# Optimization experiments

Measured on AMD Instinct MI355X. Metric: run time of the kernel, lower is better.

## Reference

```python
import jax, jax.numpy as jnp
import numpy as np

B, S, D = 2, 1024, 1024
L, E, F = 2, 8, 2048


def setup_inputs() -> dict:
    key = jax.random.key(0)
    kx, kp, k1, k2 = jax.random.split(key, 4)
    x = jax.random.normal(kx, (B, S, D), dtype=jnp.float32)
    # prototypes scaled so dot products are O(1), keeping softmax well-behaved
    protos = jax.random.normal(kp, (L, E, D), dtype=jnp.float32) / np.sqrt(D)
    W1 = jax.random.normal(k1, (L, E, D, F), dtype=jnp.float32) * 0.02
    W2 = jax.random.normal(k2, (L, E, F, D), dtype=jnp.float32) * 0.02
    return {"x": x, "protos": protos, "W1": W1, "W2": W2, "k": 2}


def _route(x, protos_l, k):
    # expert_mapping: abs(dot(prototype, input)) per expert, keep top-k, rest -> -inf, softmax
    scores = jnp.abs(jnp.einsum("bsd,ed->bse", x, protos_l))  # [B,S,E]
    topv, _ = jax.lax.top_k(scores, k)
    thresh = topv[..., -1:]  # k-th largest per token
    masked = jnp.where(scores >= thresh, scores, -jnp.inf)
    return jax.nn.softmax(masked, axis=-1)  # [B,S,E]


def reference(x, protos, W1, W2, k):
    n_layers = protos.shape[0]
    for l in range(n_layers):  # fixed small layer loop
        w = _route(x, protos[l], k)  # [B,S,E]
        h = jax.nn.relu(jnp.einsum("bsd,edf->bsef", x, W1[l]))  # [B,S,E,F]
        y = jnp.einsum("bsef,efd,bse->bsd", h, W2[l], w)  # weighted expert mix
        x = x + y
    return x
```

## Files before the change

### kernel.cpp

```cpp
#include <hip/hip_runtime.h>
#include <hip/hip_bf16.h>
#include <cstdint>

#define T_TOKENS 2048
#define DDIM 1024
#define FDIM 2048
#define NEXP 8
#define BMPAD 64
#define RMAX 4608
#define RALLOC 4736

#define ATILE_EL 2048
#define BTILE_EL 4096

typedef unsigned short u16;
typedef short bf16x8 __attribute__((ext_vector_type(8)));
typedef u16 u16x8 __attribute__((ext_vector_type(8)));
typedef u16 u16x4v __attribute__((ext_vector_type(4)));
typedef float f32x4 __attribute__((ext_vector_type(4)));

#define VMCNT(n) asm volatile("s_waitcnt vmcnt(" #n ")" ::: "memory")
#define SB() __builtin_amdgcn_sched_barrier(0)
#define BAR() __builtin_amdgcn_s_barrier()

__device__ __forceinline__ u16 bf16_rn(float f) {
  unsigned u = __builtin_bit_cast(unsigned, f);
  u += 0x7fffu + ((u >> 16) & 1u);
  return (u16)(u >> 16);
}
__device__ __forceinline__ float bf16_f(u16 h) {
  unsigned u = ((unsigned)h) << 16;
  return __builtin_bit_cast(float, u);
}
__device__ __forceinline__ void gl16(const void* g, void* l) {
  __builtin_amdgcn_global_load_lds((const __attribute__((address_space(1))) void*)g,
                                   (__attribute__((address_space(3))) void*)l, 16, 0, 0);
}

template <int GX, int GY, int GZ>
__device__ __forceinline__ void swz3(unsigned lin, int& bx, int& by, int& bz) {
  constexpr unsigned nwg = (unsigned)GX * GY * GZ;
  const unsigned nl = (lin & 7u) * (nwg >> 3) + (lin >> 3);
  bx = nl % GX;
  const unsigned t = nl / GX;
  by = t % GY;
  bz = t / GY;
}


__device__ __forceinline__ void route_dev(
    int t, const float* __restrict__ x, const float* __restrict__ protos,
    int* __restrict__ eid, float* __restrict__ wgt, float* red) {
  const int tid = threadIdx.x;
  const float4 xv = ((const float4*)(x + (size_t)t * DDIM))[tid];
  float acc[NEXP];
#pragma unroll
  for (int e = 0; e < NEXP; ++e) {
    const float4 p = ((const float4*)protos)[e * 256 + tid];
    acc[e] = xv.x * p.x + xv.y * p.y + xv.z * p.z + xv.w * p.w;
  }
#pragma unroll
  for (int e = 0; e < NEXP; ++e) red[e * 256 + tid] = acc[e];
  __syncthreads();
  for (int s = 128; s > 0; s >>= 1) {
    if (tid < s) {
#pragma unroll
      for (int e = 0; e < NEXP; ++e) red[e * 256 + tid] += red[e * 256 + tid + s];
    }
    __syncthreads();
  }
  if (tid == 0) {
    float m1 = -1.f, m2 = -1.f;
    int i1 = 0, i2 = 0;
#pragma unroll
    for (int e = 0; e < NEXP; ++e) {
      float s = fabsf(red[e * 256]);
      if (s > m1) { m2 = m1; i2 = i1; m1 = s; i1 = e; }
      else if (s > m2) { m2 = s; i2 = e; }
    }
    float e2 = __expf(m2 - m1);
    float z = 1.f + e2;
    eid[t * 2] = i1;
    eid[t * 2 + 1] = i2;
    wgt[t * 2] = 1.f / z;
    wgt[t * 2 + 1] = e2 / z;
  }
}

template <bool LO>
__device__ __forceinline__ void wconv_dev(
    int nb, int kb, int e, const float* __restrict__ W, u16* __restrict__ Hi,
    u16* __restrict__ Lo, int K, int N, float* tile) {
  const float* Wp = W + ((size_t)e * K + (size_t)kb * 32) * N + nb * 128;
  const int t = threadIdx.x;
#pragma unroll
  for (int i = 0; i < 4; ++i) {
    const int f4 = i * 256 + t;
    const int kr = f4 >> 5;
    const int c4 = (f4 & 31) * 4;
    float4 v = *(const float4*)(Wp + (size_t)kr * N + c4);
    *(float4*)&tile[kr * 129 + c4] = v;
  }
  __syncthreads();
  const size_t tb = (((size_t)e * (N >> 7) + nb) * (K >> 5) + kb) * BTILE_EL;
#pragma unroll
  for (int j = 0; j < 2; ++j) {
    const int cid = j * 256 + t;
    const int n = cid & 127, ksel = cid >> 7;
    u16x8 hv, lv;
#pragma unroll
    for (int i = 0; i < 8; ++i) {
      float f = tile[(ksel * 8 + i) * 129 + n];
      u16 h = bf16_rn(f);
      hv[i] = h;
      if (LO) lv[i] = bf16_rn(f - bf16_f(h));
    }
    *(u16x8*)(Hi + tb + (size_t)cid * 8) = hv;
    if (LO) *(u16x8*)(Lo + tb + (size_t)cid * 8) = lv;
  }
}

__device__ __forceinline__ void wconv_p_dev(
    int nb, int kb, int e, const float* __restrict__ W, u16* __restrict__ Hi,
    const float* __restrict__ proto2, float* __restrict__ Ppart, int K, int N,
    float* smem) {
  float* tile = smem;
  float* pr = smem + 32 * 129;
  const float* Wp = W + ((size_t)e * K + (size_t)kb * 32) * N + nb * 128;
  const int t = threadIdx.x;
#pragma unroll
  for (int i = 0; i < 4; ++i) {
    const int f4 = i * 256 + t;
    const int kr = f4 >> 5;
    const int c4 = (f4 & 31) * 4;
    float4 v = *(const float4*)(Wp + (size_t)kr * N + c4);
    *(float4*)&tile[kr * 129 + c4] = v;
  }
  {
    const int idx = t * 4;
    const int e2 = idx >> 7, n = idx & 127;
    *(float4*)&pr[e2 * 128 + n] =
        *(const float4*)(proto2 + (size_t)e2 * DDIM + nb * 128 + n);
  }
  __syncthreads();
  const size_t tb = (((size_t)e * (N >> 7) + nb) * (K >> 5) + kb) * BTILE_EL;
#pragma unroll
  for (int j = 0; j < 2; ++j) {
    const int cid = j * 256 + t;
    const int n = cid & 127, ksel = cid >> 7;
    u16x8 hv;
#pragma unroll
    for (int i = 0; i < 8; ++i) hv[i] = bf16_rn(tile[(ksel * 8 + i) * 129 + n]);
    *(u16x8*)(Hi + tb + (size_t)cid * 8) = hv;
  }
  const int e2 = t >> 5, f = t & 31;
  float s = 0.f;
#pragma unroll 16
  for (int n = 0; n < 128; ++n) s += tile[f * 129 + n] * pr[e2 * 128 + n];
  Ppart[(((size_t)nb * NEXP + e) * NEXP + e2) * FDIM + kb * 32 + f] = s;
}

template <bool LO>
__device__ __forceinline__ void gather_dev(
    int r, const float* __restrict__ x, const int* __restrict__ row2token,
    u16* __restrict__ Ahi, u16* __restrict__ Alo) {
  const int t = row2token[r];
  const int c = threadIdx.x * 4;
  float4 v = make_float4(0.f, 0.f, 0.f, 0.f);
  if (t >= 0) v = *(const float4*)(x + (size_t)t * DDIM + c);
  float vv[4] = {v.x, v.y, v.z, v.w};
  u16x4v hi, lo;
#pragma unroll
  for (int i = 0; i < 4; ++i) {
    u16 h = bf16_rn(vv[i]);
    hi[i] = h;
    if (LO) lo[i] = bf16_rn(vv[i] - bf16_f(h));
  }
  const size_t el = ((size_t)(r >> 6) * (DDIM >> 5) + (c >> 5)) * ATILE_EL +
                    (size_t)(((c >> 3) & 3) * 64 + (r & 63)) * 8 + (c & 7);
  *(u16x4v*)(Ahi + el) = hi;
  if (LO) *(u16x4v*)(Alo + el) = lo;
}

__device__ __forceinline__ void gemm_split_dev(
    unsigned lin, u16* lds, const u16* __restrict__ Ahi, const u16* __restrict__ Alo,
    const u16* __restrict__ Bhi, const u16* __restrict__ Blo,
    u16* __restrict__ OutHi, u16* __restrict__ OutLo,
    const int* __restrict__ cnt, const int* __restrict__ offp, int K, int N) {
  int bx, by, bz;
  swz3<FDIM / 128, RMAX / 64, NEXP>(lin, bx, by, bz);
  const int e = bz;
  const int cp = (cnt[e] + 63) & ~63;
  if (by * 64 >= cp) return;
  const int row0 = offp[e] + by * 64;
  const int n0 = bx * 128;
  const int nkb = K >> 5;
  constexpr int BUF_EL = 12288;

  const int tid = threadIdx.x;
  const int lane = tid & 63;
  const int wid = tid >> 6;
  const int wr = wid >> 1, wc = wid & 1;
  const int lr = lane & 15, kg = lane >> 4;
  const int lo16 = lane << 4;

  f32x4 acc[2][4];
#pragma unroll
  for (int i = 0; i < 2; ++i)
#pragma unroll
    for (int j = 0; j < 4; ++j)
#pragma unroll
      for (int r = 0; r < 4; ++r) acc[i][j][r] = 0.f;

  const size_t abase = (size_t)(row0 >> 6) * nkb;
  const size_t bbase = ((size_t)e * (N >> 7) + (n0 >> 7)) * nkb;

  auto STAGE = [&](int kb, int b) {
    char* d = (char*)(lds + b * BUF_EL);
    const char* gah = (const char*)(Ahi + (abase + kb) * ATILE_EL);
    const char* gal = (const char*)(Alo + (abase + kb) * ATILE_EL);
    const char* gbh = (const char*)(Bhi + (bbase + kb) * BTILE_EL);
    const char* gbl = (const char*)(Blo + (bbase + kb) * BTILE_EL);
    if (wid == 0) {
      gl16(gah + 0 * 1024 + lo16, d + 0 * 1024);
      gl16(gah + 1 * 1024 + lo16, d + 1 * 1024);
      gl16(gah + 2 * 1024 + lo16, d + 2 * 1024);
      gl16(gah + 3 * 1024 + lo16, d + 3 * 1024);
      gl16(gal + 0 * 1024 + lo16, d + 4096 + 0 * 1024);
      gl16(gal + 1 * 1024 + lo16, d + 4096 + 1 * 1024);
    } else if (wid == 1) {
      gl16(gal + 2 * 1024 + lo16, d + 4096 + 2 * 1024);
      gl16(gal + 3 * 1024 + lo16, d + 4096 + 3 * 1024);
      gl16(gbh + 0 * 1024 + lo16, d + 8192 + 0 * 1024);
      gl16(gbh + 1 * 1024 + lo16, d + 8192 + 1 * 1024);
      gl16(gbh + 2 * 1024 + lo16, d + 8192 + 2 * 1024);
      gl16(gbh + 3 * 1024 + lo16, d + 8192 + 3 * 1024);
    } else if (wid == 2) {
      gl16(gbh + 4 * 1024 + lo16, d + 8192 + 4 * 1024);
      gl16(gbh + 5 * 1024 + lo16, d + 8192 + 5 * 1024);
      gl16(gbh + 6 * 1024 + lo16, d + 8192 + 6 * 1024);
      gl16(gbh + 7 * 1024 + lo16, d + 8192 + 7 * 1024);
      gl16(gbl + 0 * 1024 + lo16, d + 16384 + 0 * 1024);
      gl16(gbl + 1 * 1024 + lo16, d + 16384 + 1 * 1024);
    } else {
      gl16(gbl + 2 * 1024 + lo16, d + 16384 + 2 * 1024);
      gl16(gbl + 3 * 1024 + lo16, d + 16384 + 3 * 1024);
      gl16(gbl + 4 * 1024 + lo16, d + 16384 + 4 * 1024);
      gl16(gbl + 5 * 1024 + lo16, d + 16384 + 5 * 1024);
      gl16(gbl + 6 * 1024 + lo16, d + 16384 + 6 * 1024);
      gl16(gbl + 7 * 1024 + lo16, d + 16384 + 7 * 1024);
    }
  };

  STAGE(0, 0);
  int cur = 0;
  for (int kb = 0; kb < nkb; ++kb) {
    const bool pf = (kb + 1 < nkb);
    if (pf) STAGE(kb + 1, cur ^ 1);
    if (pf) { VMCNT(6); } else { VMCNT(0); }
    SB(); BAR(); SB();

    const u16* buf = lds + cur * BUF_EL;
    const u16* AsH = buf;
    const u16* AsL = buf + 2048;
    const u16* BsH = buf + 4096;
    const u16* BsL = buf + 8192;
    const int arow = (kg * 64 + wr * 32 + lr) * 8;
    const int bcol = (kg * 128 + wc * 64 + lr) * 8;

    bf16x8 ah0 = *(const bf16x8*)&AsH[arow];
    bf16x8 ah1 = *(const bf16x8*)&AsH[arow + 128];
    bf16x8 bh[4];
#pragma unroll
    for (int j = 0; j < 4; ++j) bh[j] = *(const bf16x8*)&BsH[bcol + j * 128];
#pragma unroll
    for (int j = 0; j < 4; ++j) {
      acc[0][j] = __builtin_amdgcn_mfma_f32_16x16x32_bf16(ah0, bh[j], acc[0][j], 0, 0, 0);
      acc[1][j] = __builtin_amdgcn_mfma_f32_16x16x32_bf16(ah1, bh[j], acc[1][j], 0, 0, 0);
    }
    bf16x8 al0 = *(const bf16x8*)&AsL[arow];
    bf16x8 al1 = *(const bf16x8*)&AsL[arow + 128];
#pragma unroll
    for (int j = 0; j < 4; ++j) {
      bf16x8 bl = *(const bf16x8*)&BsL[bcol + j * 128];
      acc[0][j] = __builtin_amdgcn_mfma_f32_16x16x32_bf16(ah0, bl, acc[0][j], 0, 0, 0);
      acc[1][j] = __builtin_amdgcn_mfma_f32_16x16x32_bf16(ah1, bl, acc[1][j], 0, 0, 0);
      acc[0][j] = __builtin_amdgcn_mfma_f32_16x16x32_bf16(al0, bh[j], acc[0][j], 0, 0, 0);
      acc[1][j] = __builtin_amdgcn_mfma_f32_16x16x32_bf16(al1, bh[j], acc[1][j], 0, 0, 0);
    }
    SB(); BAR(); SB();
    cur ^= 1;
  }

  const int nkbO = N >> 5;
#pragma unroll
  for (int i = 0; i < 2; ++i) {
#pragma unroll
    for (int j = 0; j < 4; ++j) {
      const int Cj = n0 + wc * 64 + j * 16 + lr;
      f32x4 v = acc[i][j];
#pragma unroll
      for (int r = 0; r < 4; ++r) {
        const int R = row0 + wr * 32 + i * 16 + kg * 4 + r;
        float f = fmaxf(v[r], 0.f);
        const size_t el = ((size_t)(R >> 6) * nkbO + (Cj >> 5)) * ATILE_EL +
                          (size_t)(((Cj >> 3) & 3) * 64 + (R & 63)) * 8 + (Cj & 7);
        u16 h = bf16_rn(f);
        OutHi[el] = h;
        OutLo[el] = bf16_rn(f - bf16_f(h));
      }
    }
  }
}

template <int GX, int GY, bool RELU, int OUTMODE>
__device__ __forceinline__ void gemm_plain_dev(
    unsigned lin, u16* lds, const u16* __restrict__ Ahi, const u16* __restrict__ Bhi,
    u16* __restrict__ OutHi, float* __restrict__ OutF,
    const int* __restrict__ cnt, const int* __restrict__ offp, int K, int N) {
  int bx, by, bz;
  swz3<GX, GY, NEXP>(lin, bx, by, bz);
  const int e = bz;
  const int cp = (cnt[e] + 63) & ~63;
  if (by * 128 >= cp) return;
  const int row0 = offp[e] + by * 128;
  const int rend = offp[e] + cp;
  const int n0 = bx * 128;
  const int nkb = K >> 5;
  constexpr int BUF_EL = 8192;

  const int tid = threadIdx.x;
  const int lane = tid & 63;
  const int wid = tid >> 6;
  const int wr = wid >> 1, wc = wid & 1;
  const int lr = lane & 15, kg = lane >> 4;
  const int lo16 = lane << 4;

  f32x4 acc[4][4];
#pragma unroll
  for (int i = 0; i < 4; ++i)
#pragma unroll
    for (int j = 0; j < 4; ++j)
#pragma unroll
      for (int r = 0; r < 4; ++r) acc[i][j][r] = 0.f;

  const int at0 = row0 >> 6;
  const size_t bbase = ((size_t)e * (N >> 7) + (n0 >> 7)) * nkb;

  auto STAGE = [&](int kb, int b) {
    char* d = (char*)(lds + b * BUF_EL);
    if (wid < 2) {
      const char* g = (const char*)(Ahi + ((size_t)(at0 + wid) * nkb + kb) * ATILE_EL);
      gl16(g + 0 * 1024 + lo16, d + wid * 4096 + 0 * 1024);
      gl16(g + 1 * 1024 + lo16, d + wid * 4096 + 1 * 1024);
      gl16(g + 2 * 1024 + lo16, d + wid * 4096 + 2 * 1024);
      gl16(g + 3 * 1024 + lo16, d + wid * 4096 + 3 * 1024);
    } else {
      const char* g = (const char*)(Bhi + (bbase + kb) * BTILE_EL) + (wid - 2) * 4096;
      gl16(g + 0 * 1024 + lo16, d + 8192 + (wid - 2) * 4096 + 0 * 1024);
      gl16(g + 1 * 1024 + lo16, d + 8192 + (wid - 2) * 4096 + 1 * 1024);
      gl16(g + 2 * 1024 + lo16, d + 8192 + (wid - 2) * 4096 + 2 * 1024);
      gl16(g + 3 * 1024 + lo16, d + 8192 + (wid - 2) * 4096 + 3 * 1024);
    }
  };

  STAGE(0, 0);
  int cur = 0;
  for (int kb = 0; kb < nkb; ++kb) {
    const bool pf = (kb + 1 < nkb);
    if (pf) STAGE(kb + 1, cur ^ 1);
    if (pf) { VMCNT(4); } else { VMCNT(0); }
    SB(); BAR(); SB();

    const u16* buf = lds + cur * BUF_EL;
    const u16* AsH = buf + wr * 2048;
    const u16* BsH = buf + 4096;
    const int arow = (kg * 64 + lr) * 8;
    const int bcol = (kg * 128 + wc * 64 + lr) * 8;

    bf16x8 ah[4], bh[4];
#pragma unroll
    for (int i = 0; i < 4; ++i) ah[i] = *(const bf16x8*)&AsH[arow + i * 128];
#pragma unroll
    for (int j = 0; j < 4; ++j) bh[j] = *(const bf16x8*)&BsH[bcol + j * 128];
#pragma unroll
    for (int i = 0; i < 4; ++i)
#pragma unroll
      for (int j = 0; j < 4; ++j)
        acc[i][j] = __builtin_amdgcn_mfma_f32_16x16x32_bf16(ah[i], bh[j], acc[i][j], 0, 0, 0);
    SB(); BAR(); SB();
    cur ^= 1;
  }

  const int nkbO = N >> 5;
#pragma unroll
  for (int i = 0; i < 4; ++i) {
#pragma unroll
    for (int j = 0; j < 4; ++j) {
      const int Cj = n0 + wc * 64 + j * 16 + lr;
      f32x4 v = acc[i][j];
#pragma unroll
      for (int r = 0; r < 4; ++r) {
        const int R = row0 + wr * 64 + i * 16 + kg * 4 + r;
        if (R >= rend) continue;
        float f = v[r];
        if (RELU) f = fmaxf(f, 0.f);
        if constexpr (OUTMODE == 0) {
          OutF[(size_t)R * N + Cj] = f;
        } else {
          const size_t el = ((size_t)(R >> 6) * nkbO + (Cj >> 5)) * ATILE_EL +
                            (size_t)(((Cj >> 3) & 3) * 64 + (R & 63)) * 8 + (Cj & 7);
          OutHi[el] = bf16_rn(f);
        }
      }
    }
  }
}

__device__ __forceinline__ void compact_dev(
    const int* __restrict__ eid, int* __restrict__ cnt, int* __restrict__ offp,
    int* __restrict__ row2token, int* __restrict__ pos, int* lcnt) {
  int* s_off = lcnt + NEXP * 256;
  int* s_tot = s_off + NEXP;
  const int tid = threadIdx.x;
  const int base = tid * 16;
  int my[16];
#pragma unroll
  for (int i = 0; i < 4; ++i)
    *(int4*)&my[i * 4] = *(const int4*)(eid + base + i * 4);
#pragma unroll
  for (int e = 0; e < NEXP; ++e) {
    int c = 0;
#pragma unroll
    for (int i = 0; i < 16; ++i) c += (my[i] == e) ? 1 : 0;
    lcnt[e * 256 + tid] = c;
  }
  for (int r = tid; r < RMAX; r += 256) row2token[r] = -1;
  __syncthreads();
  if (tid < NEXP) {
    int run = 0;
    for (int i = 0; i < 256; ++i) {
      int v = lcnt[tid * 256 + i];
      lcnt[tid * 256 + i] = run;
      run += v;
    }
    s_tot[tid] = run;
  }
  __syncthreads();
  if (tid == 0) {
    int o = 0;
    for (int e = 0; e < NEXP; ++e) {
      s_off[e] = o;
      o += (s_tot[e] + BMPAD - 1) & ~(BMPAD - 1);
    }
  }
  __syncthreads();
  int myoff[NEXP];
#pragma unroll
  for (int e = 0; e < NEXP; ++e) myoff[e] = s_off[e] + lcnt[e * 256 + tid];
#pragma unroll
  for (int i = 0; i < 16; ++i) {
    int r = 0;
#pragma unroll
    for (int e = 0; e < NEXP; ++e) r = (my[i] == e) ? myoff[e] : r;
    row2token[r] = (base + i) >> 1;
    pos[base + i] = r;
#pragma unroll
    for (int e = 0; e < NEXP; ++e) myoff[e] += (my[i] == e) ? 1 : 0;
  }
  if (tid < NEXP) {
    cnt[tid] = s_tot[tid];
    offp[tid] = s_off[tid];
  }
}


__global__ __launch_bounds__(256) void fusedK1_kernel(
    const float* __restrict__ xin, const float* __restrict__ protos,
    int* __restrict__ eidA, float* __restrict__ wgtA,
    const float* __restrict__ W2, u16* __restrict__ W2A,
    const float* __restrict__ proto2, float* __restrict__ Ppart,
    const float* __restrict__ W1, u16* __restrict__ W_hi, u16* __restrict__ W_lo) {
  __shared__ float smem[32 * 129 + 8 * 128];
  const unsigned lin = blockIdx.x;
  if (lin < 2048u) {
    route_dev((int)lin, xin, protos, eidA, wgtA, smem);
  } else if (lin < 6144u) {
    const unsigned l2 = lin - 2048u;
    wconv_p_dev(l2 % 8, (l2 / 8) % 64, l2 / 512, W2, W2A, proto2, Ppart,
                FDIM, DDIM, smem);
  } else {
    const unsigned l3 = lin - 6144u;
    wconv_dev<true>(l3 % 16, (l3 / 16) % 32, l3 / 512, W1, W_hi, W_lo,
                    DDIM, FDIM, smem);
  }
}

__global__ __launch_bounds__(256) void compact_kernel(
    const int* __restrict__ eid, int* __restrict__ cnt, int* __restrict__ offp,
    int* __restrict__ row2token, int* __restrict__ pos) {
  __shared__ int lcnt[NEXP * 256 + 16];
  compact_dev(eid, cnt, offp, row2token, pos, lcnt);
}

__global__ __launch_bounds__(256) void fusedK3_kernel(
    const float* __restrict__ xin, const int* __restrict__ row2token,
    u16* __restrict__ Ag_hi, u16* __restrict__ Ag_lo,
    const float* __restrict__ Ppart, float* __restrict__ P) {
  const unsigned lin = blockIdx.x;
  if (lin < (unsigned)RMAX) {
    gather_dev<true>((int)lin, xin, row2token, Ag_hi, Ag_lo);
  } else {
    const int i = (int)(lin - RMAX) * 256 + threadIdx.x;
    float s = 0.f;
#pragma unroll
    for (int nb = 0; nb < 8; ++nb) s += Ppart[(size_t)nb * (NEXP * NEXP * FDIM) + i];
    P[i] = s;
  }
}

__global__ __launch_bounds__(256, 3) void fusedC2_kernel(
    const u16* __restrict__ Ag_hi, const u16* __restrict__ Ag_lo,
    const u16* __restrict__ W_hi, const u16* __restrict__ W_lo,
    u16* __restrict__ h_hi, u16* __restrict__ h_lo,
    const int* __restrict__ cnt, const int* __restrict__ offp) {
  __shared__ u16 lds[2 * 12288];
  gemm_split_dev(blockIdx.x, lds, Ag_hi, Ag_lo, W_hi, W_lo, h_hi, h_lo, cnt, offp,
                 DDIM, FDIM);
}

__global__ __launch_bounds__(256, 4) void fusedC3_kernel(
    const u16* __restrict__ h_hi, const u16* __restrict__ W2A,
    float* __restrict__ part, const int* __restrict__ cnt, const int* __restrict__ offp,
    const float* __restrict__ W1b, u16* __restrict__ W_lo,
    const float* __restrict__ W2b, u16* __restrict__ W_hi) {
  __shared__ u16 lds[2 * 8192];
  const unsigned lin = blockIdx.x;
  if (lin < 2304u) {
    gemm_plain_dev<DDIM / 128, RMAX / 128, false, 0>(
        lin, lds, h_hi, W2A, nullptr, part, cnt, offp, FDIM, DDIM);
  } else if (lin < 6400u) {
    const unsigned l2 = lin - 2304u;
    wconv_dev<false>(l2 % 16, (l2 / 16) % 32, l2 / 512, W1b, W_lo, nullptr,
                     DDIM, FDIM, (float*)lds);
  } else {
    const unsigned l2 = lin - 6400u;
    wconv_dev<false>(l2 % 8, (l2 / 8) % 64, l2 / 512, W2b, W_hi, nullptr,
                     FDIM, DDIM, (float*)lds);
  }
}

__global__ __launch_bounds__(256) void route2_kernel(
    const float* __restrict__ x, const float* __restrict__ protos2,
    const u16* __restrict__ h_hi, const u16* __restrict__ h_lo,
    const float* __restrict__ P, const int* __restrict__ eidA,
    const int* __restrict__ pos, const float* __restrict__ wgtA,
    int* __restrict__ eidB, float* __restrict__ wgtB) {
  const int t = blockIdx.x;
  const int tid = threadIdx.x;
  __shared__ float red[NEXP][256];
  const float4 xv = ((const float4*)(x + (size_t)t * DDIM))[tid];
  float acc[NEXP];
#pragma unroll
  for (int e = 0; e < NEXP; ++e) {
    const float4 p = ((const float4*)protos2)[e * 256 + tid];
    acc[e] = xv.x * p.x + xv.y * p.y + xv.z * p.z + xv.w * p.w;
  }
  const int p0 = pos[t * 2], p1 = pos[t * 2 + 1];
  const int e0 = eidA[t * 2], e1 = eidA[t * 2 + 1];
  const float w0 = wgtA[t * 2], w1 = wgtA[t * 2 + 1];
  const int f0 = tid * 8;
  const int nkbF = FDIM >> 5;
  float h0[8], h1[8];
  {
    const size_t el0 = ((size_t)(p0 >> 6) * nkbF + (f0 >> 5)) * ATILE_EL +
                       (size_t)((((f0 >> 3) & 3) * 64 + (p0 & 63)) * 8);
    const size_t el1 = ((size_t)(p1 >> 6) * nkbF + (f0 >> 5)) * ATILE_EL +
                       (size_t)((((f0 >> 3) & 3) * 64 + (p1 & 63)) * 8);
    u16x8 a = *(const u16x8*)&h_hi[el0], b = *(const u16x8*)&h_lo[el0];
    u16x8 c = *(const u16x8*)&h_hi[el1], d = *(const u16x8*)&h_lo[el1];
#pragma unroll
    for (int j = 0; j < 8; ++j) {
      h0[j] = bf16_f(a[j]) + bf16_f(b[j]);
      h1[j] = bf16_f(c[j]) + bf16_f(d[j]);
    }
  }
#pragma unroll
  for (int e2 = 0; e2 < NEXP; ++e2) {
    const float* P0 = P + ((size_t)(e0 * NEXP + e2)) * FDIM + f0;
    const float* P1 = P + ((size_t)(e1 * NEXP + e2)) * FDIM + f0;
    float c = 0.f;
#pragma unroll
    for (int j = 0; j < 8; ++j) c += w0 * h0[j] * P0[j] + w1 * h1[j] * P1[j];
    acc[e2] += c;
  }
#pragma unroll
  for (int e = 0; e < NEXP; ++e) red[e][tid] = acc[e];
  __syncthreads();
  for (int s = 128; s > 0; s >>= 1) {
    if (tid < s) {
#pragma unroll
      for (int e = 0; e < NEXP; ++e) red[e][tid] += red[e][tid + s];
    }
    __syncthreads();
  }
  if (tid == 0) {
    float m1 = -1.f, m2 = -1.f;
    int i1 = 0, i2 = 0;
#pragma unroll
    for (int e = 0; e < NEXP; ++e) {
      float s = fabsf(red[e][0]);
      if (s > m1) { m2 = m1; i2 = i1; m1 = s; i1 = e; }
      else if (s > m2) { m2 = s; i2 = e; }
    }
    float e2 = __expf(m2 - m1);
    float z = 1.f + e2;
    eidB[t * 2] = i1;
    eidB[t * 2 + 1] = i2;
    wgtB[t * 2] = 1.f / z;
    wgtB[t * 2 + 1] = e2 / z;
  }
}

__global__ __launch_bounds__(256) void fusedD_kernel(
    const float* __restrict__ part, const int* __restrict__ pos,
    const float* __restrict__ wgt, const float* __restrict__ xin,
    float* __restrict__ xcur,
    const int* __restrict__ eidB, int* __restrict__ cnt, int* __restrict__ offp,
    int* __restrict__ row2token, int* __restrict__ posB) {
  __shared__ int lcnt[NEXP * 256 + 16];
  const unsigned lin = blockIdx.x;
  if (lin < 2048u) {
    const int t = lin;
    const int c = threadIdx.x * 4;
    const int p0 = pos[t * 2], p1 = pos[t * 2 + 1];
    const float w0 = wgt[t * 2], w1 = wgt[t * 2 + 1];
    float4 xa = *(const float4*)(xin + (size_t)t * DDIM + c);
    const float4 y0 = *(const float4*)(part + (size_t)p0 * DDIM + c);
    const float4 y1 = *(const float4*)(part + (size_t)p1 * DDIM + c);
    xa.x += w0 * y0.x + w1 * y1.x;
    xa.y += w0 * y0.y + w1 * y1.y;
    xa.z += w0 * y0.z + w1 * y1.z;
    xa.w += w0 * y0.w + w1 * y1.w;
    *(float4*)(xcur + (size_t)t * DDIM + c) = xa;
  } else {
    compact_dev(eidB, cnt, offp, row2token, posB, lcnt);
  }
}

__global__ __launch_bounds__(256) void gather_kernel(
    const float* __restrict__ x, const int* __restrict__ row2token,
    u16* __restrict__ Ahi) {
  gather_dev<false>(blockIdx.x, x, row2token, Ahi, nullptr);
}

template <int GX, bool RELU, int OUTMODE>
__global__ __launch_bounds__(256, 4) void gemm_plain_kernel(
    const u16* __restrict__ Ahi, const u16* __restrict__ Bhi,
    u16* __restrict__ OutHi, float* __restrict__ OutF,
    const int* __restrict__ cnt, const int* __restrict__ offp, int K, int N) {
  __shared__ u16 lds[2 * 8192];
  gemm_plain_dev<GX, RMAX / 128, RELU, OUTMODE>(blockIdx.x, lds, Ahi, Bhi, OutHi,
                                                OutF, cnt, offp, K, N);
}

__global__ __launch_bounds__(256) void apply_kernel(
    const float* __restrict__ part, const int* __restrict__ pos,
    const float* __restrict__ wgt, float* __restrict__ x) {
  const int t = blockIdx.x;
  const int c = threadIdx.x * 4;
  const int p0 = pos[t * 2], p1 = pos[t * 2 + 1];
  const float w0 = wgt[t * 2], w1 = wgt[t * 2 + 1];
  float4 xa = *(float4*)(x + (size_t)t * DDIM + c);
  const float4 y0 = *(const float4*)(part + (size_t)p0 * DDIM + c);
  const float4 y1 = *(const float4*)(part + (size_t)p1 * DDIM + c);
  xa.x += w0 * y0.x + w1 * y1.x;
  xa.y += w0 * y0.y + w1 * y1.y;
  xa.z += w0 * y0.z + w1 * y1.z;
  xa.w += w0 * y0.w + w1 * y1.w;
  *(float4*)(x + (size_t)t * DDIM + c) = xa;
}

extern "C" void kernel_launch(void* const* d_in, const int* in_sizes, int n_in,
                              void* d_out, int out_size, void* d_ws, size_t ws_size,
                              hipStream_t stream) {
  const float* xin = (const float*)d_in[0];
  const float* protos = (const float*)d_in[1];
  const float* W1 = (const float*)d_in[2];
  const float* W2 = (const float*)d_in[3];
  float* xcur = (float*)d_out;

  u16* W_hi = (u16*)d_ws;
  u16* W_lo = W_hi + (size_t)NEXP * DDIM * FDIM;
  u16* W2A = W_lo + (size_t)NEXP * DDIM * FDIM;
  u16* Ag_hi = W2A + (size_t)NEXP * DDIM * FDIM;
  u16* Ag_lo = Ag_hi + (size_t)RALLOC * DDIM;
  u16* h_hi = Ag_lo + (size_t)RALLOC * DDIM;
  u16* h_lo = h_hi + (size_t)RALLOC * FDIM;
  float* part = (float*)(h_lo + (size_t)RALLOC * FDIM);
  float* Ppart = part + (size_t)RALLOC * DDIM;
  float* P = Ppart + (size_t)8 * NEXP * NEXP * FDIM;
  float* wgtA = P + (size_t)NEXP * NEXP * FDIM;
  float* wgtB = wgtA + T_TOKENS * 2;
  int* eidA = (int*)(wgtB + T_TOKENS * 2);
  int* eidB = eidA + T_TOKENS * 2;
  int* posA = eidB + T_TOKENS * 2;
  int* posB = posA + T_TOKENS * 2;
  int* cnt = posB + T_TOKENS * 2;
  int* offp = cnt + NEXP;
  int* row2token = offp + NEXP;

  const float* protos2 = protos + (size_t)NEXP * DDIM;
  const float* W1b = W1 + (size_t)NEXP * DDIM * FDIM;
  const float* W2b = W2 + (size_t)NEXP * FDIM * DDIM;

  fusedK1_kernel<<<2048 + 4096 + 4096, 256, 0, stream>>>(
      xin, protos, eidA, wgtA, W2, W2A, protos2, Ppart, W1, W_hi, W_lo);
  compact_kernel<<<1, 256, 0, stream>>>(eidA, cnt, offp, row2token, posA);
  fusedK3_kernel<<<RMAX + 512, 256, 0, stream>>>(
      xin, row2token, Ag_hi, Ag_lo, Ppart, P);
  fusedC2_kernel<<<(FDIM / 128) * (RMAX / 64) * NEXP, 256, 0, stream>>>(
      Ag_hi, Ag_lo, W_hi, W_lo, h_hi, h_lo, cnt, offp);
  fusedC3_kernel<<<2304 + 4096 + 4096, 256, 0, stream>>>(
      h_hi, W2A, part, cnt, offp, W1b, W_lo, W2b, W_hi);
  route2_kernel<<<T_TOKENS, 256, 0, stream>>>(
      xin, protos2, h_hi, h_lo, P, eidA, posA, wgtA, eidB, wgtB);
  fusedD_kernel<<<2048 + 1, 256, 0, stream>>>(
      part, posA, wgtA, xin, xcur, eidB, cnt, offp, row2token, posB);

  gather_kernel<<<RMAX, 256, 0, stream>>>(xcur, row2token, Ag_hi);
  gemm_plain_kernel<FDIM / 128, true, 2>
      <<<(FDIM / 128) * (RMAX / 128) * NEXP, 256, 0, stream>>>(
          Ag_hi, W_lo, h_hi, nullptr, cnt, offp, DDIM, FDIM);
  gemm_plain_kernel<DDIM / 128, false, 0>
      <<<(DDIM / 128) * (RMAX / 128) * NEXP, 256, 0, stream>>>(
          h_hi, W_hi, nullptr, part, cnt, offp, FDIM, DDIM);
  apply_kernel<<<T_TOKENS, 256, 0, stream>>>(part, posB, wgtB, xcur);
}
```

Before: 331.3 us.

## Fuse second-layer routing into C3 kernel and fix LDS padding in weight conversion

Moves the route2 kernel's work into extra blocks of fusedC3, removing one kernel launch and letting routing run alongside the GEMM and weight-conversion blocks. It also changes the weight-transpose LDS row pitch from 129 to 132 floats so float4 stores are aligned. The proto dot product is rewritten with float4 reads whose start index is rotated per thread to spread LDS bank accesses. Cost: the shared 16K-u16 LDS buffer (32 KB) must hold route2's 8x256 float reduction array, and fusedC3 gets more parameters and register pressure.

```diff
diff --git a/kernel.cpp b/kernel.cpp
--- a/kernel.cpp
+++ b/kernel.cpp
@@ -12,6 +12,7 @@
 
 #define ATILE_EL 2048
 #define BTILE_EL 4096
+#define WLDP 132
 
 typedef unsigned short u16;
 typedef short bf16x8 __attribute__((ext_vector_type(8)));
@@ -99,7 +100,7 @@
     const int kr = f4 >> 5;
     const int c4 = (f4 & 31) * 4;
     float4 v = *(const float4*)(Wp + (size_t)kr * N + c4);
-    *(float4*)&tile[kr * 129 + c4] = v;
+    *(float4*)&tile[kr * WLDP + c4] = v;
   }
   __syncthreads();
   const size_t tb = (((size_t)e * (N >> 7) + nb) * (K >> 5) + kb) * BTILE_EL;
@@ -110,7 +111,7 @@
     u16x8 hv, lv;
 #pragma unroll
     for (int i = 0; i < 8; ++i) {
-      float f = tile[(ksel * 8 + i) * 129 + n];
+      float f = tile[(ksel * 8 + i) * WLDP + n];
       u16 h = bf16_rn(f);
       hv[i] = h;
       if (LO) lv[i] = bf16_rn(f - bf16_f(h));
@@ -125,7 +126,7 @@
     const float* __restrict__ proto2, float* __restrict__ Ppart, int K, int N,
     float* smem) {
   float* tile = smem;
-  float* pr = smem + 32 * 129;
+  float* pr = smem + 32 * WLDP;
   const float* Wp = W + ((size_t)e * K + (size_t)kb * 32) * N + nb * 128;
   const int t = threadIdx.x;
 #pragma unroll
@@ -134,7 +135,7 @@
     const int kr = f4 >> 5;
     const int c4 = (f4 & 31) * 4;
     float4 v = *(const float4*)(Wp + (size_t)kr * N + c4);
-    *(float4*)&tile[kr * 129 + c4] = v;
+    *(float4*)&tile[kr * WLDP + c4] = v;
   }
   {
     const int idx = t * 4;
@@ -150,13 +151,18 @@
     const int n = cid & 127, ksel = cid >> 7;
     u16x8 hv;
 #pragma unroll
-    for (int i = 0; i < 8; ++i) hv[i] = bf16_rn(tile[(ksel * 8 + i) * 129 + n]);
+    for (int i = 0; i < 8; ++i) hv[i] = bf16_rn(tile[(ksel * 8 + i) * WLDP + n]);
     *(u16x8*)(Hi + tb + (size_t)cid * 8) = hv;
   }
   const int e2 = t >> 5, f = t & 31;
   float s = 0.f;
-#pragma unroll 16
-  for (int n = 0; n < 128; ++n) s += tile[f * 129 + n] * pr[e2 * 128 + n];
+#pragma unroll
+  for (int ii = 0; ii < 32; ++ii) {
+    const int n4 = ((ii + f) & 31) * 4;
+    const float4 tv = *(const float4*)&tile[f * WLDP + n4];
+    const float4 pv = *(const float4*)&pr[e2 * 128 + n4];
+    s += tv.x * pv.x + tv.y * pv.y + tv.z * pv.z + tv.w * pv.w;
+  }
   Ppart[(((size_t)nb * NEXP + e) * NEXP + e2) * FDIM + kb * 32 + f] = s;
 }
 
@@ -180,6 +186,76 @@
                     (size_t)(((c >> 3) & 3) * 64 + (r & 63)) * 8 + (c & 7);
   *(u16x4v*)(Ahi + el) = hi;
   if (LO) *(u16x4v*)(Alo + el) = lo;
+}
+
+__device__ __forceinline__ void route2_dev(
+    int t, const float* __restrict__ x, const float* __restrict__ protos2,
+    const u16* __restrict__ h_hi, const u16* __restrict__ h_lo,
+    const float* __restrict__ P, const int* __restrict__ eidA,
+    const int* __restrict__ pos, const float* __restrict__ wgtA,
+    int* __restrict__ eidB, float* __restrict__ wgtB, float* red) {
+  const int tid = threadIdx.x;
+  const float4 xv = ((const float4*)(x + (size_t)t * DDIM))[tid];
+  float acc[NEXP];
+#pragma unroll
+  for (int e = 0; e < NEXP; ++e) {
+    const float4 p = ((const float4*)protos2)[e * 256 + tid];
+    acc[e] = xv.x * p.x + xv.y * p.y + xv.z * p.z + xv.w * p.w;
+  }
+  const int p0 = pos[t * 2], p1 = pos[t * 2 + 1];
+  const int e0 = eidA[t * 2], e1 = eidA[t * 2 + 1];
+  const float w0 = wgtA[t * 2], w1 = wgtA[t * 2 + 1];
+  const int f0 = tid * 8;
+  const int nkbF = FDIM >> 5;
+  float h0[8], h1[8];
+  {
+    const size_t el0 = ((size_t)(p0 >> 6) * nkbF + (f0 >> 5)) * ATILE_EL +
+                       (size_t)((((f0 >> 3) & 3) * 64 + (p0 & 63)) * 8);
+    const size_t el1 = ((size_t)(p1 >> 6) * nkbF + (f0 >> 5)) * ATILE_EL +
+                       (size_t)((((f0 >> 3) & 3) * 64 + (p1 & 63)) * 8);
+    u16x8 a = *(const u16x8*)&h_hi[el0], b = *(const u16x8*)&h_lo[el0];
+    u16x8 c = *(const u16x8*)&h_hi[el1], d = *(const u16x8*)&h_lo[el1];
+#pragma unroll
+    for (int j = 0; j < 8; ++j) {
+      h0[j] = bf16_f(a[j]) + bf16_f(b[j]);
+      h1[j] = bf16_f(c[j]) + bf16_f(d[j]);
+    }
+  }
+#pragma unroll
+  for (int e2 = 0; e2 < NEXP; ++e2) {
+    const float* P0 = P + ((size_t)(e0 * NEXP + e2)) * FDIM + f0;
+    const float* P1 = P + ((size_t)(e1 * NEXP + e2)) * FDIM + f0;
+    float c = 0.f;
+#pragma unroll
+    for (int j = 0; j < 8; ++j) c += w0 * h0[j] * P0[j] + w1 * h1[j] * P1[j];
+    acc[e2] += c;
+  }
+#pragma unroll
+  for (int e = 0; e < NEXP; ++e) red[e * 256 + tid] = acc[e];
+  __syncthreads();
+  for (int s = 128; s > 0; s >>= 1) {
+    if (tid < s) {
+#pragma unroll
+      for (int e = 0; e < NEXP; ++e) red[e * 256 + tid] += red[e * 256 + tid + s];
+    }
+    __syncthreads();
+  }
+  if (tid == 0) {
+    float m1 = -1.f, m2 = -1.f;
+    int i1 = 0, i2 = 0;
+#pragma unroll
+    for (int e = 0; e < NEXP; ++e) {
+      float s = fabsf(red[e * 256]);
+      if (s > m1) { m2 = m1; i2 = i1; m1 = s; i1 = e; }
+      else if (s > m2) { m2 = s; i2 = e; }
+    }
+    float e2 = __expf(m2 - m1);
+    float z = 1.f + e2;
+    eidB[t * 2] = i1;
+    eidB[t * 2 + 1] = i2;
+    wgtB[t * 2] = 1.f / z;
+    wgtB[t * 2 + 1] = e2 / z;
+  }
 }
 
 __device__ __forceinline__ void gemm_split_dev(
@@ -481,7 +557,7 @@
     const float* __restrict__ W2, u16* __restrict__ W2A,
     const float* __restrict__ proto2, float* __restrict__ Ppart,
     const float* __restrict__ W1, u16* __restrict__ W_hi, u16* __restrict__ W_lo) {
-  __shared__ float smem[32 * 129 + 8 * 128];
+  __shared__ float smem[32 * WLDP + 8 * 128];
   const unsigned lin = blockIdx.x;
   if (lin < 2048u) {
     route_dev((int)lin, xin, protos, eidA, wgtA, smem);
@@ -530,10 +606,15 @@
 }
 
 __global__ __launch_bounds__(256, 4) void fusedC3_kernel(
-    const u16* __restrict__ h_hi, const u16* __restrict__ W2A,
+    const u16* __restrict__ h_hi, const u16* __restrict__ h_lo,
+    const u16* __restrict__ W2A,
     float* __restrict__ part, const int* __restrict__ cnt, const int* __restrict__ offp,
     const float* __restrict__ W1b, u16* __restrict__ W_lo,
-    const float* __restrict__ W2b, u16* __restrict__ W_hi) {
+    const float* __restrict__ W2b, u16* __restrict__ W_hi,
+    const float* __restrict__ xin, const float* __restrict__ protos2,
+    const float* __restrict__ P, const int* __restrict__ eidA,
+    const int* __restrict__ posA, const float* __restrict__ wgtA,
+    int* __restrict__ eidB, float* __restrict__ wgtB) {
   __shared__ u16 lds[2 * 8192];
   const unsigned lin = blockIdx.x;
   if (lin < 2304u) {
@@ -543,82 +624,13 @@
     const unsigned l2 = lin - 2304u;
     wconv_dev<false>(l2 % 16, (l2 / 16) % 32, l2 / 512, W1b, W_lo, nullptr,
                      DDIM, FDIM, (float*)lds);
-  } else {
+  } else if (lin < 10496u) {
     const unsigned l2 = lin - 6400u;
     wconv_dev<false>(l2 % 8, (l2 / 8) % 64, l2 / 512, W2b, W_hi, nullptr,
                      FDIM, DDIM, (float*)lds);
-  }
-}
-
-__global__ __launch_bounds__(256) void route2_kernel(
-    const float* __restrict__ x, const float* __restrict__ protos2,
-    const u16* __restrict__ h_hi, const u16* __restrict__ h_lo,
-    const float* __restrict__ P, const int* __restrict__ eidA,
-    const int* __restrict__ pos, const float* __restrict__ wgtA,
-    int* __restrict__ eidB, float* __restrict__ wgtB) {
-  const int t = blockIdx.x;
-  const int tid = threadIdx.x;
-  __shared__ float red[NEXP][256];
-  const float4 xv = ((const float4*)(x + (size_t)t * DDIM))[tid];
-  float acc[NEXP];
-#pragma unroll
-  for (int e = 0; e < NEXP; ++e) {
-    const float4 p = ((const float4*)protos2)[e * 256 + tid];
-    acc[e] = xv.x * p.x + xv.y * p.y + xv.z * p.z + xv.w * p.w;
-  }
-  const int p0 = pos[t * 2], p1 = pos[t * 2 + 1];
-  const int e0 = eidA[t * 2], e1 = eidA[t * 2 + 1];
-  const float w0 = wgtA[t * 2], w1 = wgtA[t * 2 + 1];
-  const int f0 = tid * 8;
-  const int nkbF = FDIM >> 5;
-  float h0[8], h1[8];
-  {
-    const size_t el0 = ((size_t)(p0 >> 6) * nkbF + (f0 >> 5)) * ATILE_EL +
-                       (size_t)((((f0 >> 3) & 3) * 64 + (p0 & 63)) * 8);
-    const size_t el1 = ((size_t)(p1 >> 6) * nkbF + (f0 >> 5)) * ATILE_EL +
-                       (size_t)((((f0 >> 3) & 3) * 64 + (p1 & 63)) * 8);
-    u16x8 a = *(const u16x8*)&h_hi[el0], b = *(const u16x8*)&h_lo[el0];
-    u16x8 c = *(const u16x8*)&h_hi[el1], d = *(const u16x8*)&h_lo[el1];
-#pragma unroll
-    for (int j = 0; j < 8; ++j) {
-      h0[j] = bf16_f(a[j]) + bf16_f(b[j]);
-      h1[j] = bf16_f(c[j]) + bf16_f(d[j]);
-    }
-  }
-#pragma unroll
-  for (int e2 = 0; e2 < NEXP; ++e2) {
-    const float* P0 = P + ((size_t)(e0 * NEXP + e2)) * FDIM + f0;
-    const float* P1 = P + ((size_t)(e1 * NEXP + e2)) * FDIM + f0;
-    float c = 0.f;
-#pragma unroll
-    for (int j = 0; j < 8; ++j) c += w0 * h0[j] * P0[j] + w1 * h1[j] * P1[j];
-    acc[e2] += c;
-  }
-#pragma unroll
-  for (int e = 0; e < NEXP; ++e) red[e][tid] = acc[e];
-  __syncthreads();
-  for (int s = 128; s > 0; s >>= 1) {
-    if (tid < s) {
-#pragma unroll
-      for (int e = 0; e < NEXP; ++e) red[e][tid] += red[e][tid + s];
-    }
-    __syncthreads();
-  }
-  if (tid == 0) {
-    float m1 = -1.f, m2 = -1.f;
-    int i1 = 0, i2 = 0;
-#pragma unroll
-    for (int e = 0; e < NEXP; ++e) {
-      float s = fabsf(red[e][0]);
-      if (s > m1) { m2 = m1; i2 = i1; m1 = s; i1 = e; }
-      else if (s > m2) { m2 = s; i2 = e; }
-    }
-    float e2 = __expf(m2 - m1);
-    float z = 1.f + e2;
-    eidB[t * 2] = i1;
-    eidB[t * 2 + 1] = i2;
-    wgtB[t * 2] = 1.f / z;
-    wgtB[t * 2 + 1] = e2 / z;
+  } else {
+    route2_dev((int)(lin - 10496u), xin, protos2, h_hi, h_lo, P, eidA, posA, wgtA,
+               eidB, wgtB, (float*)lds);
   }
 }
 
@@ -721,10 +733,9 @@
       xin, row2token, Ag_hi, Ag_lo, Ppart, P);
   fusedC2_kernel<<<(FDIM / 128) * (RMAX / 64) * NEXP, 256, 0, stream>>>(
       Ag_hi, Ag_lo, W_hi, W_lo, h_hi, h_lo, cnt, offp);
-  fusedC3_kernel<<<2304 + 4096 + 4096, 256, 0, stream>>>(
-      h_hi, W2A, part, cnt, offp, W1b, W_lo, W2b, W_hi);
-  route2_kernel<<<T_TOKENS, 256, 0, stream>>>(
-      xin, protos2, h_hi, h_lo, P, eidA, posA, wgtA, eidB, wgtB);
+  fusedC3_kernel<<<2304 + 4096 + 4096 + 2048, 256, 0, stream>>>(
+      h_hi, h_lo, W2A, part, cnt, offp, W1b, W_lo, W2b, W_hi,
+      xin, protos2, P, eidA, posA, wgtA, eidB, wgtB);
   fusedD_kernel<<<2048 + 1, 256, 0, stream>>>(
       part, posA, wgtA, xin, xcur, eidB, cnt, offp, row2token, posB);
 
```

Result: faster. 315.3 us (-4.8%).
